# Optimization experiments

Hardware: AMD Instinct MI355X
Metric: run time of the kernel (lower is better)

The kernel has to match this reference:

```python
import jax, jax.numpy as jnp
import numpy as np
import math

EMBED = 1024
HEADS = 16
HEAD_DIM = EMBED // HEADS
B, S = 2, 2048


def setup_inputs() -> dict:
    key = jax.random.key(0)
    ks = jax.random.split(key, 11)
    s = 1.0 / math.sqrt(EMBED)
    return {
        "query": jax.random.normal(ks[0], (B, S, EMBED), jnp.float32),
        "key_": jax.random.normal(ks[1], (B, S, EMBED), jnp.float32),
        "value": jax.random.normal(ks[2], (B, S, EMBED), jnp.float32),
        "Wq": jax.random.normal(ks[3], (EMBED, EMBED), jnp.float32) * s,
        "bq": jax.random.normal(ks[4], (EMBED,), jnp.float32) * s,
        "Wk": jax.random.normal(ks[5], (EMBED, EMBED), jnp.float32) * s,
        "bk": jax.random.normal(ks[6], (EMBED,), jnp.float32) * s,
        "Wv": jax.random.normal(ks[7], (EMBED, EMBED), jnp.float32) * s,
        "bv": jax.random.normal(ks[8], (EMBED,), jnp.float32) * s,
        "Wo": jax.random.normal(ks[9], (EMBED, EMBED), jnp.float32) * s,
        "bo": jax.random.normal(ks[10], (EMBED,), jnp.float32) * s,
    }


def reference(query, key_, value, Wq, bq, Wk, bk, Wv, bv, Wo, bo):
    b, s, e = query.shape
    # projections (torch Linear: x @ W.T + b)
    q = query @ Wq.T + bq
    k = key_ @ Wk.T + bk
    v = value @ Wv.T + bv
    # [B, H, S, hd]
    q = q.reshape(b, s, HEADS, HEAD_DIM).transpose(0, 2, 1, 3)
    k = k.reshape(b, s, HEADS, HEAD_DIM).transpose(0, 2, 1, 3)
    v = v.reshape(b, s, HEADS, HEAD_DIM).transpose(0, 2, 1, 3)
    scores = jnp.einsum("bhqd,bhkd->bhqk", q, k) / math.sqrt(HEAD_DIM)
    attn = jax.nn.softmax(scores, axis=-1)
    out = jnp.einsum("bhqk,bhkd->bhqd", attn, v)
    out = out.transpose(0, 2, 1, 3).reshape(b, s, e)
    return out @ Wo.T + bo
```

## Files before the change

kernel.cpp:

```cpp
#include <hip/hip_runtime.h>
#include <hip/hip_bf16.h>

using bf16_t = __bf16;
using bf16x2 = __attribute__((ext_vector_type(2))) __bf16;
using bf16x4 = __attribute__((ext_vector_type(4))) __bf16;
using bf16x8 = __attribute__((ext_vector_type(8))) __bf16;
using f32x4  = __attribute__((ext_vector_type(4))) float;
using u32 = unsigned int;
using u32x4 = __attribute__((ext_vector_type(4))) u32;
using i32x2 = __attribute__((ext_vector_type(2))) int;

constexpr int S_ = 2048, E_ = 1024, M_ = 4096;
constexpr size_t MAT_A = (size_t)M_ * E_;
constexpr size_t MAT_W = (size_t)E_ * E_;

__device__ __forceinline__ bf16_t tobf(float f) {
  unsigned u = __builtin_bit_cast(unsigned, f);
  unsigned short r = (unsigned short)((u + 0x7fffu + ((u >> 16) & 1u)) >> 16);
  return __builtin_bit_cast(bf16_t, r);
}
__device__ __forceinline__ u32 packbf2(float a, float b) {
  u32 ua = __builtin_bit_cast(u32, a) + 0x8000u;
  u32 ub = __builtin_bit_cast(u32, b) + 0x8000u;
  return (ua >> 16) | (ub & 0xffff0000u);
}
__device__ __forceinline__ u32 cvtpk(float lo, float hi) {
  bf16x2 t;
  t[0] = (bf16_t)lo;
  t[1] = (bf16_t)hi;
  return __builtin_bit_cast(u32, t);
}
__device__ __forceinline__ void swap32(u32& a, u32& b) {
  i32x2 r = __builtin_amdgcn_permlane32_swap((int)a, (int)b, false, false);
  a = (u32)r[0];
  b = (u32)r[1];
}
__device__ __forceinline__ void swap16(u32& a, u32& b) {
  i32x2 r = __builtin_amdgcn_permlane16_swap((int)a, (int)b, false, false);
  a = (u32)r[0];
  b = (u32)r[1];
}
__device__ __forceinline__ void async_lds16(const bf16_t* g, bf16_t* l) {
  __builtin_amdgcn_global_load_lds(
      (const __attribute__((address_space(1))) unsigned int*)g,
      (__attribute__((address_space(3))) unsigned int*)l, 16, 0, 0);
}

__global__ __launch_bounds__(256) void cvt_all(
    const float* __restrict__ s0, const float* __restrict__ s1,
    const float* __restrict__ s2, const float* __restrict__ s3,
    const float* __restrict__ s4, const float* __restrict__ s5,
    const float* __restrict__ s6,
    bf16_t* __restrict__ d0, bf16_t* __restrict__ d1,
    bf16_t* __restrict__ d2, bf16_t* __restrict__ d3,
    bf16_t* __restrict__ d4, bf16_t* __restrict__ d5,
    bf16_t* __restrict__ d6) {
  size_t i8 = ((size_t)blockIdx.x * 256 + threadIdx.x) * 8;
  const float* s;
  bf16_t* d;
  size_t off;
  if (i8 < 3 * MAT_A) {
    int w = (int)(i8 >> 22);
    off = i8 & (MAT_A - 1);
    s = w == 0 ? s0 : w == 1 ? s1 : s2;
    d = w == 0 ? d0 : w == 1 ? d1 : d2;
  } else {
    size_t j = i8 - 3 * MAT_A;
    int w = (int)(j >> 20);
    off = j & (MAT_W - 1);
    s = w == 0 ? s3 : w == 1 ? s4 : w == 2 ? s5 : s6;
    d = w == 0 ? d3 : w == 1 ? d4 : w == 2 ? d5 : d6;
  }
  float4 a = *(const float4*)(s + off);
  float4 b = *(const float4*)(s + off + 4);
  bf16x8 o;
  o[0] = tobf(a.x); o[1] = tobf(a.y); o[2] = tobf(a.z); o[3] = tobf(a.w);
  o[4] = tobf(b.x); o[5] = tobf(b.y); o[6] = tobf(b.z); o[7] = tobf(b.w);
  *(bf16x8*)(d + off) = o;
}

__global__ __launch_bounds__(256) void gemm_qkv(
    const bf16_t* __restrict__ xq, const bf16_t* __restrict__ xk,
    const bf16_t* __restrict__ xv, const bf16_t* __restrict__ wq,
    const bf16_t* __restrict__ wk, const bf16_t* __restrict__ wv,
    const float* __restrict__ bq, const float* __restrict__ bk,
    const float* __restrict__ bv, bf16_t* __restrict__ outb,
    bf16_t* __restrict__ Vt) {
  constexpr int K = 1024, N = 1024, BK = 64;
  constexpr float SC = 0.18033688011f;
  __shared__ __align__(16) bf16_t smem[2][16384];

  const int which = blockIdx.y >> 3;
  const bf16_t* X = which == 0 ? xq : which == 1 ? xk : xv;
  const bf16_t* W = which == 0 ? wq : which == 1 ? wk : wv;
  const float* bias = which == 0 ? bq : which == 1 ? bk : bv;
  const int row0 = blockIdx.x * 128, col0 = (blockIdx.y & 7) * 128;

  const int tid = threadIdx.x, lane = tid & 63, wave = tid >> 6;
  const int l15 = lane & 15, q = lane >> 4;
  const int wm = (wave & 1) * 64, wn = (wave >> 1) * 64;
  const f32x4 fzero = {0.f, 0.f, 0.f, 0.f};

  f32x4 acc[4][4];
#pragma unroll
  for (int i = 0; i < 4; ++i)
#pragma unroll
    for (int j = 0; j < 4; ++j) acc[i][j] = fzero;

  const int srow = lane >> 3;
  const int schunk = ((lane & 7) ^ srow) * 8;
  const bf16_t* gA = X + (size_t)(row0 + wave * 32 + srow) * K + schunk;
  const bf16_t* gB = W + (size_t)(col0 + wave * 32 + srow) * K + schunk;
  const int lofs = wave * 32 * BK;

  int ck[2];
  ck[0] = ((q) ^ (l15 & 7)) * 8;
  ck[1] = ((4 + q) ^ (l15 & 7)) * 8;

#pragma unroll
  for (int p = 0; p < 4; ++p) {
    async_lds16(gA + (size_t)(p * 8) * K, smem[0] + lofs + p * 8 * BK);
    async_lds16(gB + (size_t)(p * 8) * K, smem[0] + 8192 + lofs + p * 8 * BK);
  }

  for (int it = 0; it < 16; ++it) {
    const int cur = it & 1;
    __syncthreads();
    if (it + 1 < 16) {
      const int k1 = (it + 1) * BK;
      bf16_t* dA = smem[cur ^ 1] + lofs;
      bf16_t* dB = smem[cur ^ 1] + 8192 + lofs;
#pragma unroll
      for (int p = 0; p < 4; ++p) {
        async_lds16(gA + k1 + (size_t)(p * 8) * K, dA + p * 8 * BK);
        async_lds16(gB + k1 + (size_t)(p * 8) * K, dB + p * 8 * BK);
      }
    }
    const bf16_t* As = smem[cur];
    const bf16_t* Bs = smem[cur] + 8192;
#pragma unroll
    for (int h = 0; h < 2; ++h) {
      bf16x8 af[4], bw[4];
#pragma unroll
      for (int i = 0; i < 4; ++i)
        af[i] = *(const bf16x8*)(As + (wm + i * 16 + l15) * BK + ck[h]);
#pragma unroll
      for (int j = 0; j < 4; ++j)
        bw[j] = *(const bf16x8*)(Bs + (wn + j * 16 + l15) * BK + ck[h]);
#pragma unroll
      for (int i = 0; i < 4; ++i)
#pragma unroll
        for (int j = 0; j < 4; ++j)
          acc[i][j] = __builtin_amdgcn_mfma_f32_16x16x32_bf16(af[i], bw[j],
                                                              acc[i][j], 0, 0, 0);
    }
  }

  if (which < 2) {
    const float sc = which == 0 ? SC : 1.0f;
    bf16_t* C = outb + (size_t)which * MAT_A;
#pragma unroll
    for (int j = 0; j < 4; ++j) {
      const int col = col0 + wn + j * 16 + l15;
      const float bc = bias[col];
#pragma unroll
      for (int i = 0; i < 4; ++i)
#pragma unroll
        for (int r = 0; r < 4; ++r) {
          const int row = row0 + wm + i * 16 + q * 4 + r;
          C[(size_t)row * N + col] = tobf((acc[i][j][r] + bc) * sc);
        }
    }
  } else {
    __syncthreads();
    bf16_t* Ep = &smem[0][0] + wave * 4608;
#pragma unroll
    for (int j = 0; j < 4; ++j) {
      const float bc = bias[col0 + wn + j * 16 + l15];
      const int nl = j * 16 + l15;
#pragma unroll
      for (int i = 0; i < 4; ++i) {
        uint2 pk;
        pk.x = packbf2(acc[i][j][0] + bc, acc[i][j][1] + bc);
        pk.y = packbf2(acc[i][j][2] + bc, acc[i][j][3] + bc);
        *(uint2*)(Ep + nl * 72 + i * 16 + q * 4) = pk;
      }
    }
    const int head = (col0 + wn) >> 6;
    const int tok0 = row0 + wm;
    const int bb = tok0 >> 11, tokb = tok0 & 2047;
    const int dl = lane >> 3, ml = (lane & 7) * 8;
#pragma unroll
    for (int p = 0; p < 8; ++p) {
      const int d = dl + p * 8;
      bf16x8 v = *(const bf16x8*)(Ep + d * 72 + ml);
      *(bf16x8*)(Vt + ((size_t)((bb * 16 + head) * 64 + d)) * S_ + tokb + ml) = v;
    }
  }
}

__global__ __launch_bounds__(256) void gemm_o(const bf16_t* __restrict__ X,
                                              const bf16_t* __restrict__ W,
                                              const float* __restrict__ bias,
                                              float* __restrict__ C) {
  constexpr int K = 1024, N = 1024, BK = 64;
  __shared__ __align__(16) bf16_t smem[2][12288];
  const int tid = threadIdx.x, lane = tid & 63, wave = tid >> 6;
  const int l15 = lane & 15, q = lane >> 4;
  const int row0 = blockIdx.x * 64, col0 = blockIdx.y * 128;
  const int wm = (wave & 1) * 32, wn = (wave >> 1) * 64;
  const f32x4 fzero = {0.f, 0.f, 0.f, 0.f};

  f32x4 acc[2][4];
#pragma unroll
  for (int i = 0; i < 2; ++i)
#pragma unroll
    for (int j = 0; j < 4; ++j) acc[i][j] = fzero;

  const int srow = lane >> 3;
  const int schunk = ((lane & 7) ^ srow) * 8;
  const bf16_t* gA = X + (size_t)(row0 + wave * 16 + srow) * K + schunk;
  const bf16_t* gB = W + (size_t)(col0 + wave * 32 + srow) * K + schunk;
  const int lofsA = wave * 16 * BK;
  const int lofsB = wave * 32 * BK;

  int ck[2];
  ck[0] = ((q) ^ (l15 & 7)) * 8;
  ck[1] = ((4 + q) ^ (l15 & 7)) * 8;

  async_lds16(gA, smem[0] + lofsA);
  async_lds16(gA + (size_t)8 * K, smem[0] + lofsA + 8 * BK);
#pragma unroll
  for (int p = 0; p < 4; ++p)
    async_lds16(gB + (size_t)(p * 8) * K, smem[0] + 4096 + lofsB + p * 8 * BK);

  for (int it = 0; it < 16; ++it) {
    const int cur = it & 1;
    __syncthreads();
    if (it + 1 < 16) {
      const int k1 = (it + 1) * BK;
      bf16_t* dA = smem[cur ^ 1] + lofsA;
      bf16_t* dB = smem[cur ^ 1] + 4096 + lofsB;
      async_lds16(gA + k1, dA);
      async_lds16(gA + k1 + (size_t)8 * K, dA + 8 * BK);
#pragma unroll
      for (int p = 0; p < 4; ++p)
        async_lds16(gB + k1 + (size_t)(p * 8) * K, dB + p * 8 * BK);
    }
    const bf16_t* As = smem[cur];
    const bf16_t* Bs = smem[cur] + 4096;
#pragma unroll
    for (int h = 0; h < 2; ++h) {
      bf16x8 af[2], bw[4];
#pragma unroll
      for (int i = 0; i < 2; ++i)
        af[i] = *(const bf16x8*)(As + (wm + i * 16 + l15) * BK + ck[h]);
#pragma unroll
      for (int j = 0; j < 4; ++j)
        bw[j] = *(const bf16x8*)(Bs + (wn + j * 16 + l15) * BK + ck[h]);
#pragma unroll
      for (int i = 0; i < 2; ++i)
#pragma unroll
        for (int j = 0; j < 4; ++j)
          acc[i][j] = __builtin_amdgcn_mfma_f32_16x16x32_bf16(af[i], bw[j],
                                                              acc[i][j], 0, 0, 0);
    }
  }

#pragma unroll
  for (int j = 0; j < 4; ++j) {
    const int col = col0 + wn + j * 16 + l15;
    const float bc = bias[col];
#pragma unroll
    for (int i = 0; i < 2; ++i)
#pragma unroll
      for (int r = 0; r < 4; ++r) {
        const int row = row0 + wm + i * 16 + q * 4 + r;
        C[(size_t)row * N + col] = acc[i][j][r] + bc;
      }
  }
}

__global__ __launch_bounds__(512, 4) void attn_mfma(
    const bf16_t* __restrict__ Qm, const bf16_t* __restrict__ Km,
    const bf16_t* __restrict__ Vtg, bf16_t* __restrict__ Om) {
  __shared__ __align__(16) bf16_t Ks[2][2][64 * 64];
  __shared__ __align__(16) bf16_t Vs[2][2][64 * 64];

  const int tid = threadIdx.x, lane = tid & 63, wave = tid >> 6;
  const int g = wave >> 2, wv = wave & 3;
  const int l15 = lane & 15, q = lane >> 4;
  const int bh = blockIdx.x & 31, qb = blockIdx.x >> 5;
  const int b = bh >> 4, h = bh & 15;
  const size_t rowbase = (size_t)b * S_;
  const int hcol = h * 64;
  const int q0 = qb * 128 + wv * 32;

  const int srow = lane >> 3;
  const int schunk = (lane & 7) ^ srow;
  const bf16_t* gK = Km + (rowbase + wv * 16 + srow) * E_ + hcol + schunk * 8;
  const bf16_t* gV = Vtg + ((size_t)bh * 64 + wv * 16 + srow) * S_ + schunk * 8;

  bf16x8 qf[2][2];
#pragma unroll
  for (int qt = 0; qt < 2; ++qt) {
    const bf16_t* qp = Qm + (rowbase + q0 + qt * 16 + l15) * E_ + hcol + q * 8;
    qf[qt][0] = *(const bf16x8*)qp;
    qf[qt][1] = *(const bf16x8*)(qp + 32);
  }

  bf16x8 onesv;
#pragma unroll
  for (int j = 0; j < 8; ++j)
    onesv[j] = __builtin_bit_cast(bf16_t, (unsigned short)0x3F80);

  const f32x4 fzero = {0.f, 0.f, 0.f, 0.f};
  f32x4 oacc[2][4];
#pragma unroll
  for (int qt = 0; qt < 2; ++qt)
#pragma unroll
    for (int mt = 0; mt < 4; ++mt) oacc[qt][mt] = fzero;
  f32x4 lsacc[2] = {fzero, fzero};

  const int rbase = l15 * 64;
  int ck[2];
  ck[0] = ((q) ^ (l15 & 7)) * 8;
  ck[1] = ((4 + q) ^ (l15 & 7)) * 8;

  auto STAGE = [&](int tile, int bi) {
    const size_t koff = (size_t)(tile * 64) * E_;
    const int voff = tile * 64;
    bf16_t* dK = Ks[g][bi] + wv * 1024;
    bf16_t* dV = Vs[g][bi] + wv * 1024;
    async_lds16(gK + koff, dK);
    async_lds16(gK + koff + (size_t)8 * E_, dK + 512);
    async_lds16(gV + voff, dV);
    async_lds16(gV + voff + (size_t)8 * S_, dV + 512);
  };

  auto COMPUTE = [&](const bf16_t* Kbuf, const bf16_t* Vbuf) {
    u32 uu[2][4][2];
#pragma unroll
    for (int nt = 0; nt < 4; ++nt) {
      bf16x8 a0 = *(const bf16x8*)(Kbuf + nt * 1024 + rbase + ck[0]);
      bf16x8 a1 = *(const bf16x8*)(Kbuf + nt * 1024 + rbase + ck[1]);
#pragma unroll
      for (int qt = 0; qt < 2; ++qt) {
        f32x4 st = fzero;
        st = __builtin_amdgcn_mfma_f32_16x16x32_bf16(a0, qf[qt][0], st, 0, 0, 0);
        st = __builtin_amdgcn_mfma_f32_16x16x32_bf16(a1, qf[qt][1], st, 0, 0, 0);
        uu[qt][nt][0] =
            cvtpk(__builtin_amdgcn_exp2f(st[0]), __builtin_amdgcn_exp2f(st[1]));
        uu[qt][nt][1] =
            cvtpk(__builtin_amdgcn_exp2f(st[2]), __builtin_amdgcn_exp2f(st[3]));
      }
    }
#pragma unroll
    for (int kk = 0; kk < 2; ++kk) {
      bf16x8 bp[2];
#pragma unroll
      for (int qt = 0; qt < 2; ++qt) {
        u32 A = uu[qt][2 * kk][0], Bv = uu[qt][2 * kk][1];
        u32 C = uu[qt][2 * kk + 1][0], D = uu[qt][2 * kk + 1][1];
        swap32(A, C);  swap16(A, C);
        swap32(Bv, D); swap16(Bv, D);
        u32x4 w = {A, Bv, C, D};
        bp[qt] = __builtin_bit_cast(bf16x8, w);
        lsacc[qt] = __builtin_amdgcn_mfma_f32_16x16x32_bf16(onesv, bp[qt],
                                                            lsacc[qt], 0, 0, 0);
      }
      __builtin_amdgcn_s_setprio(1);
#pragma unroll
      for (int mt = 0; mt < 4; ++mt) {
        bf16x8 av = *(const bf16x8*)(Vbuf + mt * 1024 + rbase + ck[kk]);
        oacc[0][mt] = __builtin_amdgcn_mfma_f32_16x16x32_bf16(av, bp[0],
                                                              oacc[0][mt], 0, 0, 0);
        oacc[1][mt] = __builtin_amdgcn_mfma_f32_16x16x32_bf16(av, bp[1],
                                                              oacc[1][mt], 0, 0, 0);
      }
      __builtin_amdgcn_s_setprio(0);
    }
  };

  STAGE(g, 0);
  for (int r = 0; r < 16; ++r) {
    __syncthreads();
    if (r + 1 < 16) STAGE(2 * (r + 1) + g, (r + 1) & 1);
    COMPUTE(Ks[g][r & 1], Vs[g][r & 1]);
  }

  __syncthreads();
  float* obuf = (float*)(&Ks[0][0][0]);
  float* lbuf = (float*)(&Vs[0][0][0]);
  if (g == 1) {
    float* ow = obuf + wv * 2048;
#pragma unroll
    for (int qt = 0; qt < 2; ++qt)
#pragma unroll
      for (int mt = 0; mt < 4; ++mt)
#pragma unroll
        for (int r4 = 0; r4 < 4; ++r4)
          ow[(((qt * 4 + mt) * 4) + r4) * 64 + lane] = oacc[qt][mt][r4];
    lbuf[wv * 128 + lane] = lsacc[0][0];
    lbuf[wv * 128 + 64 + lane] = lsacc[1][0];
  }
  __syncthreads();
  if (g == 0) {
    float* ow = obuf + wv * 2048;
#pragma unroll
    for (int qt = 0; qt < 2; ++qt)
#pragma unroll
      for (int mt = 0; mt < 4; ++mt)
#pragma unroll
        for (int r4 = 0; r4 < 4; ++r4)
          oacc[qt][mt][r4] += ow[(((qt * 4 + mt) * 4) + r4) * 64 + lane];
    float lsum[2];
    lsum[0] = lsacc[0][0] + lbuf[wv * 128 + lane];
    lsum[1] = lsacc[1][0] + lbuf[wv * 128 + 64 + lane];
#pragma unroll
    for (int qt = 0; qt < 2; ++qt) {
      const float inv = 1.0f / lsum[qt];
      const size_t orow = (rowbase + q0 + qt * 16 + l15) * E_ + hcol + q * 4;
#pragma unroll
      for (int mt = 0; mt < 4; ++mt) {
        bf16x4 o;
#pragma unroll
        for (int r = 0; r < 4; ++r) o[r] = tobf(oacc[qt][mt][r] * inv);
        *(bf16x4*)(Om + orow + mt * 16) = o;
      }
    }
  }
}

extern "C" void kernel_launch(void* const* d_in, const int* in_sizes, int n_in,
                              void* d_out, int out_size, void* d_ws, size_t ws_size,
                              hipStream_t stream) {
  const float* query = (const float*)d_in[0];
  const float* key_  = (const float*)d_in[1];
  const float* value = (const float*)d_in[2];
  const float* Wq = (const float*)d_in[3];
  const float* bq = (const float*)d_in[4];
  const float* Wk = (const float*)d_in[5];
  const float* bk = (const float*)d_in[6];
  const float* Wv = (const float*)d_in[7];
  const float* bv = (const float*)d_in[8];
  const float* Wo = (const float*)d_in[9];
  const float* bo = (const float*)d_in[10];

  bf16_t* qc  = (bf16_t*)d_ws;
  bf16_t* kc  = qc + MAT_A;
  bf16_t* vc  = kc + MAT_A;
  bf16_t* wqb = vc + MAT_A;
  bf16_t* wkb = wqb + MAT_W;
  bf16_t* wvb = wkb + MAT_W;
  bf16_t* wob = wvb + MAT_W;
  bf16_t* Qb  = wob + MAT_W;
  bf16_t* Kb  = Qb + MAT_A;
  bf16_t* Vt  = Kb + MAT_A;
  bf16_t* AOb = Vt + MAT_A;

  cvt_all<<<8192, 256, 0, stream>>>(query, key_, value, Wq, Wk, Wv, Wo,
                                    qc, kc, vc, wqb, wkb, wvb, wob);
  gemm_qkv<<<dim3(32, 24), 256, 0, stream>>>(qc, kc, vc, wqb, wkb, wvb,
                                             bq, bk, bv, Qb, Vt);
  attn_mfma<<<512, 512, 0, stream>>>(Qb, Kb, Vt, AOb);
  gemm_o<<<dim3(64, 8), 256, 0, stream>>>(AOb, wob, bo, (float*)d_out);
}
```

Measured before the change: 202.2 us.

## Fuse fp32-to-bf16 conversion of QKV inputs into the projection GEMM loads

Drops the separate conversion pass over the three activation tensors and the Q/K/V weights. The QKV GEMM now reads fp32 tiles from global memory into registers, converts them to bf16 and writes them into the swizzled LDS layout after the MFMA block, giving a register-staged double buffer. Only Wo is still converted by a small standalone kernel. This saves a full read/write round trip through memory and one launch, at the cost of twice the bytes per GEMM tile load, the loss of async global-to-LDS loads, and extra VGPRs and VALU work inside the GEMM loop.

```diff
diff --git a/kernel.cpp b/kernel.cpp
--- a/kernel.cpp
+++ b/kernel.cpp
@@ -46,43 +46,21 @@
       (__attribute__((address_space(3))) unsigned int*)l, 16, 0, 0);
 }
 
-__global__ __launch_bounds__(256) void cvt_all(
-    const float* __restrict__ s0, const float* __restrict__ s1,
-    const float* __restrict__ s2, const float* __restrict__ s3,
-    const float* __restrict__ s4, const float* __restrict__ s5,
-    const float* __restrict__ s6,
-    bf16_t* __restrict__ d0, bf16_t* __restrict__ d1,
-    bf16_t* __restrict__ d2, bf16_t* __restrict__ d3,
-    bf16_t* __restrict__ d4, bf16_t* __restrict__ d5,
-    bf16_t* __restrict__ d6) {
-  size_t i8 = ((size_t)blockIdx.x * 256 + threadIdx.x) * 8;
-  const float* s;
-  bf16_t* d;
-  size_t off;
-  if (i8 < 3 * MAT_A) {
-    int w = (int)(i8 >> 22);
-    off = i8 & (MAT_A - 1);
-    s = w == 0 ? s0 : w == 1 ? s1 : s2;
-    d = w == 0 ? d0 : w == 1 ? d1 : d2;
-  } else {
-    size_t j = i8 - 3 * MAT_A;
-    int w = (int)(j >> 20);
-    off = j & (MAT_W - 1);
-    s = w == 0 ? s3 : w == 1 ? s4 : w == 2 ? s5 : s6;
-    d = w == 0 ? d3 : w == 1 ? d4 : w == 2 ? d5 : d6;
-  }
-  float4 a = *(const float4*)(s + off);
-  float4 b = *(const float4*)(s + off + 4);
+__global__ __launch_bounds__(256) void cvt_wo(const float* __restrict__ s,
+                                              bf16_t* __restrict__ d) {
+  size_t i = ((size_t)blockIdx.x * 256 + threadIdx.x) * 8;
+  float4 a = *(const float4*)(s + i);
+  float4 b = *(const float4*)(s + i + 4);
   bf16x8 o;
   o[0] = tobf(a.x); o[1] = tobf(a.y); o[2] = tobf(a.z); o[3] = tobf(a.w);
   o[4] = tobf(b.x); o[5] = tobf(b.y); o[6] = tobf(b.z); o[7] = tobf(b.w);
-  *(bf16x8*)(d + off) = o;
+  *(bf16x8*)(d + i) = o;
 }
 
 __global__ __launch_bounds__(256) void gemm_qkv(
-    const bf16_t* __restrict__ xq, const bf16_t* __restrict__ xk,
-    const bf16_t* __restrict__ xv, const bf16_t* __restrict__ wq,
-    const bf16_t* __restrict__ wk, const bf16_t* __restrict__ wv,
+    const float* __restrict__ xq, const float* __restrict__ xk,
+    const float* __restrict__ xv, const float* __restrict__ wq,
+    const float* __restrict__ wk, const float* __restrict__ wv,
     const float* __restrict__ bq, const float* __restrict__ bk,
     const float* __restrict__ bv, bf16_t* __restrict__ outb,
     bf16_t* __restrict__ Vt) {
@@ -91,8 +69,8 @@
   __shared__ __align__(16) bf16_t smem[2][16384];
 
   const int which = blockIdx.y >> 3;
-  const bf16_t* X = which == 0 ? xq : which == 1 ? xk : xv;
-  const bf16_t* W = which == 0 ? wq : which == 1 ? wk : wv;
+  const float* X = which == 0 ? xq : which == 1 ? xk : xv;
+  const float* W = which == 0 ? wq : which == 1 ? wk : wv;
   const float* bias = which == 0 ? bq : which == 1 ? bk : bv;
   const int row0 = blockIdx.x * 128, col0 = (blockIdx.y & 7) * 128;
 
@@ -109,33 +87,49 @@
 
   const int srow = lane >> 3;
   const int schunk = ((lane & 7) ^ srow) * 8;
-  const bf16_t* gA = X + (size_t)(row0 + wave * 32 + srow) * K + schunk;
-  const bf16_t* gB = W + (size_t)(col0 + wave * 32 + srow) * K + schunk;
+  const float* gA = X + (size_t)(row0 + wave * 32 + srow) * K + schunk;
+  const float* gB = W + (size_t)(col0 + wave * 32 + srow) * K + schunk;
   const int lofs = wave * 32 * BK;
 
   int ck[2];
   ck[0] = ((q) ^ (l15 & 7)) * 8;
   ck[1] = ((4 + q) ^ (l15 & 7)) * 8;
 
-#pragma unroll
-  for (int p = 0; p < 4; ++p) {
-    async_lds16(gA + (size_t)(p * 8) * K, smem[0] + lofs + p * 8 * BK);
-    async_lds16(gB + (size_t)(p * 8) * K, smem[0] + 8192 + lofs + p * 8 * BK);
-  }
+  float4 ra[8], rb[8];
+  auto LOAD = [&](int k0) {
+#pragma unroll
+    for (int p = 0; p < 4; ++p) {
+      const float* sa = gA + k0 + (size_t)(p * 8) * K;
+      ra[2 * p] = *(const float4*)sa;
+      ra[2 * p + 1] = *(const float4*)(sa + 4);
+      const float* sb = gB + k0 + (size_t)(p * 8) * K;
+      rb[2 * p] = *(const float4*)sb;
+      rb[2 * p + 1] = *(const float4*)(sb + 4);
+    }
+  };
+  auto CVTW = [&](int buf) {
+#pragma unroll
+    for (int p = 0; p < 4; ++p) {
+      u32x4 wa = {cvtpk(ra[2 * p].x, ra[2 * p].y),
+                  cvtpk(ra[2 * p].z, ra[2 * p].w),
+                  cvtpk(ra[2 * p + 1].x, ra[2 * p + 1].y),
+                  cvtpk(ra[2 * p + 1].z, ra[2 * p + 1].w)};
+      *(u32x4*)(smem[buf] + lofs + p * 8 * BK + lane * 8) = wa;
+      u32x4 wb = {cvtpk(rb[2 * p].x, rb[2 * p].y),
+                  cvtpk(rb[2 * p].z, rb[2 * p].w),
+                  cvtpk(rb[2 * p + 1].x, rb[2 * p + 1].y),
+                  cvtpk(rb[2 * p + 1].z, rb[2 * p + 1].w)};
+      *(u32x4*)(smem[buf] + 8192 + lofs + p * 8 * BK + lane * 8) = wb;
+    }
+  };
+
+  LOAD(0);
+  CVTW(0);
 
   for (int it = 0; it < 16; ++it) {
     const int cur = it & 1;
     __syncthreads();
-    if (it + 1 < 16) {
-      const int k1 = (it + 1) * BK;
-      bf16_t* dA = smem[cur ^ 1] + lofs;
-      bf16_t* dB = smem[cur ^ 1] + 8192 + lofs;
-#pragma unroll
-      for (int p = 0; p < 4; ++p) {
-        async_lds16(gA + k1 + (size_t)(p * 8) * K, dA + p * 8 * BK);
-        async_lds16(gB + k1 + (size_t)(p * 8) * K, dB + p * 8 * BK);
-      }
-    }
+    if (it + 1 < 16) LOAD((it + 1) * BK);
     const bf16_t* As = smem[cur];
     const bf16_t* Bs = smem[cur] + 8192;
 #pragma unroll
@@ -154,6 +148,7 @@
           acc[i][j] = __builtin_amdgcn_mfma_f32_16x16x32_bf16(af[i], bw[j],
                                                               acc[i][j], 0, 0, 0);
     }
+    if (it + 1 < 16) CVTW(cur ^ 1);
   }
 
   if (which < 2) {
@@ -447,21 +442,14 @@
   const float* Wo = (const float*)d_in[9];
   const float* bo = (const float*)d_in[10];
 
-  bf16_t* qc  = (bf16_t*)d_ws;
-  bf16_t* kc  = qc + MAT_A;
-  bf16_t* vc  = kc + MAT_A;
-  bf16_t* wqb = vc + MAT_A;
-  bf16_t* wkb = wqb + MAT_W;
-  bf16_t* wvb = wkb + MAT_W;
-  bf16_t* wob = wvb + MAT_W;
-  bf16_t* Qb  = wob + MAT_W;
+  bf16_t* Qb  = (bf16_t*)d_ws;
   bf16_t* Kb  = Qb + MAT_A;
   bf16_t* Vt  = Kb + MAT_A;
   bf16_t* AOb = Vt + MAT_A;
-
-  cvt_all<<<8192, 256, 0, stream>>>(query, key_, value, Wq, Wk, Wv, Wo,
-                                    qc, kc, vc, wqb, wkb, wvb, wob);
-  gemm_qkv<<<dim3(32, 24), 256, 0, stream>>>(qc, kc, vc, wqb, wkb, wvb,
+  bf16_t* wob = AOb + MAT_A;
+
+  cvt_wo<<<512, 256, 0, stream>>>(Wo, wob);
+  gemm_qkv<<<dim3(32, 24), 256, 0, stream>>>(query, key_, value, Wq, Wk, Wv,
                                              bq, bk, bv, Qb, Vt);
   attn_mfma<<<512, 512, 0, stream>>>(Qb, Kb, Vt, AOb);
   gemm_o<<<dim3(64, 8), 256, 0, stream>>>(AOb, wob, bo, (float*)d_out);
```

Result: slower. 222.6 us (+10.1%).

## Double query rows per attention wave to reuse K/V tiles across more queries

Applied to the files above, without the earlier changes.

Each wave now handles 64 query rows (four 16-row tiles) instead of 32, so every block covers 256 queries and the grid halves to 256 blocks. Each K/V tile staged in LDS feeds twice as many MFMAs, which cuts global and LDS traffic per query. The cross-group reduction of partial outputs is split into two passes so it still fits the reused LDS buffers. The cost is roughly double the accumulator and score registers per wave, so launch bounds drop to 2 blocks per CU. With only 256 blocks, fewer waves are available to hide latency.

```diff
diff --git a/kernel.cpp b/kernel.cpp
--- a/kernel.cpp
+++ b/kernel.cpp
@@ -281,7 +281,7 @@
   }
 }
 
-__global__ __launch_bounds__(512, 4) void attn_mfma(
+__global__ __launch_bounds__(512, 2) void attn_mfma(
     const bf16_t* __restrict__ Qm, const bf16_t* __restrict__ Km,
     const bf16_t* __restrict__ Vtg, bf16_t* __restrict__ Om) {
   __shared__ __align__(16) bf16_t Ks[2][2][64 * 64];
@@ -294,16 +294,16 @@
   const int b = bh >> 4, h = bh & 15;
   const size_t rowbase = (size_t)b * S_;
   const int hcol = h * 64;
-  const int q0 = qb * 128 + wv * 32;
+  const int q0 = qb * 256 + wv * 64;
 
   const int srow = lane >> 3;
   const int schunk = (lane & 7) ^ srow;
   const bf16_t* gK = Km + (rowbase + wv * 16 + srow) * E_ + hcol + schunk * 8;
   const bf16_t* gV = Vtg + ((size_t)bh * 64 + wv * 16 + srow) * S_ + schunk * 8;
 
-  bf16x8 qf[2][2];
-#pragma unroll
-  for (int qt = 0; qt < 2; ++qt) {
+  bf16x8 qf[4][2];
+#pragma unroll
+  for (int qt = 0; qt < 4; ++qt) {
     const bf16_t* qp = Qm + (rowbase + q0 + qt * 16 + l15) * E_ + hcol + q * 8;
     qf[qt][0] = *(const bf16x8*)qp;
     qf[qt][1] = *(const bf16x8*)(qp + 32);
@@ -315,12 +315,12 @@
     onesv[j] = __builtin_bit_cast(bf16_t, (unsigned short)0x3F80);
 
   const f32x4 fzero = {0.f, 0.f, 0.f, 0.f};
-  f32x4 oacc[2][4];
-#pragma unroll
-  for (int qt = 0; qt < 2; ++qt)
+  f32x4 oacc[4][4];
+#pragma unroll
+  for (int qt = 0; qt < 4; ++qt)
 #pragma unroll
     for (int mt = 0; mt < 4; ++mt) oacc[qt][mt] = fzero;
-  f32x4 lsacc[2] = {fzero, fzero};
+  f32x4 lsacc[4] = {fzero, fzero, fzero, fzero};
 
   const int rbase = l15 * 64;
   int ck[2];
@@ -339,13 +339,13 @@
   };
 
   auto COMPUTE = [&](const bf16_t* Kbuf, const bf16_t* Vbuf) {
-    u32 uu[2][4][2];
+    u32 uu[4][4][2];
 #pragma unroll
     for (int nt = 0; nt < 4; ++nt) {
       bf16x8 a0 = *(const bf16x8*)(Kbuf + nt * 1024 + rbase + ck[0]);
       bf16x8 a1 = *(const bf16x8*)(Kbuf + nt * 1024 + rbase + ck[1]);
 #pragma unroll
-      for (int qt = 0; qt < 2; ++qt) {
+      for (int qt = 0; qt < 4; ++qt) {
         f32x4 st = fzero;
         st = __builtin_amdgcn_mfma_f32_16x16x32_bf16(a0, qf[qt][0], st, 0, 0, 0);
         st = __builtin_amdgcn_mfma_f32_16x16x32_bf16(a1, qf[qt][1], st, 0, 0, 0);
@@ -357,9 +357,9 @@
     }
 #pragma unroll
     for (int kk = 0; kk < 2; ++kk) {
-      bf16x8 bp[2];
-#pragma unroll
-      for (int qt = 0; qt < 2; ++qt) {
+      bf16x8 bp[4];
+#pragma unroll
+      for (int qt = 0; qt < 4; ++qt) {
         u32 A = uu[qt][2 * kk][0], Bv = uu[qt][2 * kk][1];
         u32 C = uu[qt][2 * kk + 1][0], D = uu[qt][2 * kk + 1][1];
         swap32(A, C);  swap16(A, C);
@@ -373,10 +373,10 @@
 #pragma unroll
       for (int mt = 0; mt < 4; ++mt) {
         bf16x8 av = *(const bf16x8*)(Vbuf + mt * 1024 + rbase + ck[kk]);
-        oacc[0][mt] = __builtin_amdgcn_mfma_f32_16x16x32_bf16(av, bp[0],
-                                                              oacc[0][mt], 0, 0, 0);
-        oacc[1][mt] = __builtin_amdgcn_mfma_f32_16x16x32_bf16(av, bp[1],
-                                                              oacc[1][mt], 0, 0, 0);
+#pragma unroll
+        for (int qt = 0; qt < 4; ++qt)
+          oacc[qt][mt] = __builtin_amdgcn_mfma_f32_16x16x32_bf16(
+              av, bp[qt], oacc[qt][mt], 0, 0, 0);
       }
       __builtin_amdgcn_s_setprio(0);
     }
@@ -392,43 +392,42 @@
   __syncthreads();
   float* obuf = (float*)(&Ks[0][0][0]);
   float* lbuf = (float*)(&Vs[0][0][0]);
-  if (g == 1) {
-    float* ow = obuf + wv * 2048;
-#pragma unroll
-    for (int qt = 0; qt < 2; ++qt)
-#pragma unroll
-      for (int mt = 0; mt < 4; ++mt)
-#pragma unroll
-        for (int r4 = 0; r4 < 4; ++r4)
-          ow[(((qt * 4 + mt) * 4) + r4) * 64 + lane] = oacc[qt][mt][r4];
-    lbuf[wv * 128 + lane] = lsacc[0][0];
-    lbuf[wv * 128 + 64 + lane] = lsacc[1][0];
-  }
-  __syncthreads();
-  if (g == 0) {
-    float* ow = obuf + wv * 2048;
-#pragma unroll
-    for (int qt = 0; qt < 2; ++qt)
-#pragma unroll
-      for (int mt = 0; mt < 4; ++mt)
-#pragma unroll
-        for (int r4 = 0; r4 < 4; ++r4)
-          oacc[qt][mt][r4] += ow[(((qt * 4 + mt) * 4) + r4) * 64 + lane];
-    float lsum[2];
-    lsum[0] = lsacc[0][0] + lbuf[wv * 128 + lane];
-    lsum[1] = lsacc[1][0] + lbuf[wv * 128 + 64 + lane];
-#pragma unroll
-    for (int qt = 0; qt < 2; ++qt) {
-      const float inv = 1.0f / lsum[qt];
-      const size_t orow = (rowbase + q0 + qt * 16 + l15) * E_ + hcol + q * 4;
-#pragma unroll
-      for (int mt = 0; mt < 4; ++mt) {
-        bf16x4 o;
-#pragma unroll
-        for (int r = 0; r < 4; ++r) o[r] = tobf(oacc[qt][mt][r] * inv);
-        *(bf16x4*)(Om + orow + mt * 16) = o;
-      }
-    }
+#pragma unroll
+  for (int pass = 0; pass < 2; ++pass) {
+    if (g == 1) {
+      float* ow = obuf + wv * 2048;
+#pragma unroll
+      for (int j = 0; j < 2; ++j) {
+        const int qt = pass * 2 + j;
+#pragma unroll
+        for (int mt = 0; mt < 4; ++mt)
+#pragma unroll
+          for (int r4 = 0; r4 < 4; ++r4)
+            ow[(((j * 4 + mt) * 4) + r4) * 64 + lane] = oacc[qt][mt][r4];
+        lbuf[wv * 128 + j * 64 + lane] = lsacc[qt][0];
+      }
+    }
+    __syncthreads();
+    if (g == 0) {
+      float* ow = obuf + wv * 2048;
+#pragma unroll
+      for (int j = 0; j < 2; ++j) {
+        const int qt = pass * 2 + j;
+        const float lsum = lsacc[qt][0] + lbuf[wv * 128 + j * 64 + lane];
+        const float inv = 1.0f / lsum;
+        const size_t orow = (rowbase + q0 + qt * 16 + l15) * E_ + hcol + q * 4;
+#pragma unroll
+        for (int mt = 0; mt < 4; ++mt) {
+          bf16x4 o;
+#pragma unroll
+          for (int r = 0; r < 4; ++r)
+            o[r] = tobf((oacc[qt][mt][r] +
+                         ow[(((j * 4 + mt) * 4) + r) * 64 + lane]) * inv);
+          *(bf16x4*)(Om + orow + mt * 16) = o;
+        }
+      }
+    }
+    __syncthreads();
   }
 }
 
@@ -463,6 +462,6 @@
                                     qc, kc, vc, wqb, wkb, wvb, wob);
   gemm_qkv<<<dim3(32, 24), 256, 0, stream>>>(qc, kc, vc, wqb, wkb, wvb,
                                              bq, bk, bv, Qb, Vt);
-  attn_mfma<<<512, 512, 0, stream>>>(Qb, Kb, Vt, AOb);
+  attn_mfma<<<256, 512, 0, stream>>>(Qb, Kb, Vt, AOb);
   gemm_o<<<dim3(64, 8), 256, 0, stream>>>(AOb, wob, bo, (float*)d_out);
 }
```

Result: no change. 202.3 us (+0.0%).
